# Kernel optimization log

Measured on AMD Instinct MI355X. Metric: run time of the kernel, lower is better.

Reference implementation:

```python
import jax, jax.numpy as jnp
import numpy as np

D_MODEL = 512
NUM_HEADS = 8
HEAD_DIM = D_MODEL // NUM_HEADS
B, L = 2, 4096


def setup_inputs() -> dict:
    key = jax.random.key(0)
    ks = jax.random.split(key, 7)
    query = jax.random.normal(ks[0], (B, L, D_MODEL), dtype=jnp.float32)
    k_in = jax.random.normal(ks[1], (B, L, D_MODEL), dtype=jnp.float32)
    value = jax.random.normal(ks[2], (B, L, D_MODEL), dtype=jnp.float32)
    # causal mask: True = masked (future positions)
    mask = jnp.triu(jnp.ones((L, L), dtype=jnp.bool_), k=1)
    s = 1.0 / np.sqrt(D_MODEL)
    Wq = jax.random.normal(ks[3], (D_MODEL, D_MODEL), dtype=jnp.float32) * s
    Wk = jax.random.normal(ks[4], (D_MODEL, D_MODEL), dtype=jnp.float32) * s
    Wv = jax.random.normal(ks[5], (D_MODEL, D_MODEL), dtype=jnp.float32) * s
    Wo = jax.random.normal(ks[6], (D_MODEL, D_MODEL), dtype=jnp.float32) * s
    return {"query": query, "key": k_in, "value": value, "mask": mask,
            "Wq": Wq, "Wk": Wk, "Wv": Wv, "Wo": Wo}


def reference(query, key, value, mask, Wq, Wk, Wv, Wo):
    b = query.shape[0]
    # torch nn.Linear: y = x @ W.T (no bias)
    q = query @ Wq.T
    k = key @ Wk.T
    v = value @ Wv.T
    q = q.reshape(b, -1, NUM_HEADS, HEAD_DIM)
    k = k.reshape(b, -1, NUM_HEADS, HEAD_DIM)
    v = v.reshape(b, -1, NUM_HEADS, HEAD_DIM)
    logits = jnp.einsum('bqhd,bkhd->bhqk', q, k)  # (B,H,L,L)
    logits = jnp.where(mask, -jnp.inf, logits)
    # NOTE: original scales by 1/sqrt(d_model) (not head_dim), after masking
    attn = jax.nn.softmax(logits / np.sqrt(D_MODEL).astype(np.float32), axis=3)
    out = jnp.einsum('bhqv,bvhd->bqhd', attn, v).reshape(b, -1, D_MODEL)
    return out
```

## Files before the change

kernel.cpp:

```cpp
#include <hip/hip_runtime.h>
#include <hip/hip_bf16.h>
#include <cstdint>

#define DEVI static __device__ __forceinline__

typedef __bf16 bf16x8 __attribute__((ext_vector_type(8)));
typedef float f32x4 __attribute__((ext_vector_type(4)));
typedef float f32x16 __attribute__((ext_vector_type(16)));
typedef unsigned short u16x8 __attribute__((ext_vector_type(8)));

constexpr int Bb = 2, Ll = 4096, Dd = 512, Hh = 8;
constexpr int Mm = Bb * Ll;
constexpr float SCALE2 = 1.4426950408889634f / 22.627416997969522f;
constexpr float MFIX = 16.0f;

constexpr int PITCH = 72;
constexpr int PITCHB = 144;

DEVI unsigned short f2b(float x) {
  __hip_bfloat16 h = __float2bfloat16(x);
  return *reinterpret_cast<unsigned short*>(&h);
}

DEVI float nexp2(float x) { return __builtin_amdgcn_exp2f(x); }

DEVI unsigned cvtpk(float lo, float hi) {
  unsigned r;
  asm("v_cvt_pk_bf16_f32 %0, %1, %2" : "=v"(r) : "v"(lo), "v"(hi));
  return r;
}

DEVI void gll16(const void* g, void* l) {
  __builtin_amdgcn_global_load_lds((const __attribute__((address_space(1))) void*)g,
                                   (__attribute__((address_space(3))) void*)l, 16, 0, 0);
}

__global__ void __launch_bounds__(256, 2) gemm_qkv(const float* __restrict__ Xq,
                                                   const float* __restrict__ Xk,
                                                   const float* __restrict__ Xv,
                                                   const float* __restrict__ Wqp,
                                                   const float* __restrict__ Wkp,
                                                   const float* __restrict__ Wvp,
                                                   unsigned short* __restrict__ Cb,
                                                   unsigned short* __restrict__ VtOut) {
  __shared__ __align__(16) unsigned short As[128 * PITCH];
  __shared__ __align__(16) unsigned short Bs[128 * PITCH];
  const int t = threadIdx.x, lane = t & 63;
  const int w = t >> 6, wm = w >> 1, wn = w & 1;
  const int c = lane & 15, g = lane >> 4;
  const int z = blockIdx.y;
  const float* A = (z == 0) ? Xq : (z == 1) ? Xk : Xv;
  const float* W = (z == 0) ? Wqp : (z == 1) ? Wkp : Wvp;
  const int tm = (blockIdx.x >> 2) * 128;
  const int tn = (blockIdx.x & 3) * 128;
  const int r0 = t >> 3, c8 = t & 7;

  f32x4 acc[4][4] = {};
  for (int k0 = 0; k0 < Dd; k0 += 64) {
#pragma unroll
    for (int u = 0; u < 4; ++u) {
      int r = u * 32 + r0;
      const float4* ap = reinterpret_cast<const float4*>(A + (size_t)(tm + r) * Dd + k0 + c8 * 8);
      const float4* wp = reinterpret_cast<const float4*>(W + (size_t)(tn + r) * Dd + k0 + c8 * 8);
      float4 a0 = ap[0], a1 = ap[1];
      float4 w0 = wp[0], w1 = wp[1];
      uint4 av = make_uint4(cvtpk(a0.x, a0.y), cvtpk(a0.z, a0.w),
                            cvtpk(a1.x, a1.y), cvtpk(a1.z, a1.w));
      uint4 wv = make_uint4(cvtpk(w0.x, w0.y), cvtpk(w0.z, w0.w),
                            cvtpk(w1.x, w1.y), cvtpk(w1.z, w1.w));
      *reinterpret_cast<uint4*>((char*)As + r * PITCHB + c8 * 16) = av;
      *reinterpret_cast<uint4*>((char*)Bs + r * PITCHB + c8 * 16) = wv;
    }
    __syncthreads();
#pragma unroll
    for (int kk = 0; kk < 2; ++kk) {
      bf16x8 af[4], bfv[4];
#pragma unroll
      for (int mi = 0; mi < 4; ++mi) {
        int row = wm * 64 + mi * 16 + c;
        af[mi] = *reinterpret_cast<const bf16x8*>(
            (const char*)As + row * PITCHB + kk * 64 + g * 16);
      }
#pragma unroll
      for (int ni = 0; ni < 4; ++ni) {
        int row = wn * 64 + ni * 16 + c;
        bfv[ni] = *reinterpret_cast<const bf16x8*>(
            (const char*)Bs + row * PITCHB + kk * 64 + g * 16);
      }
#pragma unroll
      for (int mi = 0; mi < 4; ++mi)
#pragma unroll
        for (int ni = 0; ni < 4; ++ni)
          acc[mi][ni] = __builtin_amdgcn_mfma_f32_16x16x32_bf16(af[mi], bfv[ni], acc[mi][ni], 0, 0, 0);
    }
    __syncthreads();
  }
  if (z == 2) {
#pragma unroll
    for (int mi = 0; mi < 4; ++mi) {
      int row0 = tm + wm * 64 + mi * 16 + g * 4;
      int bb = row0 >> 12, l = row0 & 4095;
#pragma unroll
      for (int ni = 0; ni < 4; ++ni) {
        int col = tn + wn * 64 + c + ni * 16;
        uint2 pk = make_uint2(cvtpk(acc[mi][ni][0], acc[mi][ni][1]),
                              cvtpk(acc[mi][ni][2], acc[mi][ni][3]));
        *reinterpret_cast<uint2*>(VtOut + (size_t)(bb * 512 + col) * Ll + l) = pk;
      }
    }
  } else {
    const float scl = (z == 0) ? SCALE2 : 1.0f;
    unsigned short* C = Cb + (size_t)z * (Mm * Dd);
#pragma unroll
    for (int mi = 0; mi < 4; ++mi)
#pragma unroll
      for (int j = 0; j < 4; ++j) {
        size_t row = (size_t)(tm + wm * 64 + mi * 16 + g * 4 + j);
        size_t base = row * Dd + tn + wn * 64 + c;
#pragma unroll
        for (int ni = 0; ni < 4; ++ni) C[base + ni * 16] = f2b(acc[mi][ni][j] * scl);
      }
  }
}

__global__ void __launch_bounds__(256, 2)
attn_kernel(const unsigned short* __restrict__ Q,
            const unsigned short* __restrict__ K,
            const unsigned short* __restrict__ Vt,
            float* __restrict__ O) {
  __shared__ __align__(16) char smem[65536];
  const int t = threadIdx.x, lane = t & 63, w = t >> 6;
  const int g = w >> 1, wq = w & 1;
  const int lq = lane & 31, hi = lane >> 5;
  const int bidx = blockIdx.x;
  const int xg = bidx & 7, rr = bidx >> 3;
  const int half = rr & 1, idx = rr >> 1;
  const int bh = 2 * xg + half;
  const int qi = 63 - idx;
  const int q0 = qi * 64;
  const int b = bh >> 3, h = bh & 7;

  const int qbase = q0 + wq * 32;
  const int qlane = qbase + lq;

  const unsigned short* Qrow = Q + (size_t)(b * Ll + qlane) * Dd + h * 64;
  bf16x8 qf[4];
#pragma unroll
  for (int s = 0; s < 4; ++s)
    qf[s] = *reinterpret_cast<const bf16x8*>(Qrow + s * 16 + hi * 8);

  f32x16 oacc[2] = {};
  float s_r = 0.f;

  const size_t kgbase = (size_t)(b * Ll) * Dd + h * 64;
  const size_t vgbase = (size_t)(bh * 64) * Ll;
  const int nt = qi + 1;
  const int Tg = (nt + 1) >> 1;
  const int kt0 = g * Tg;
  const int lastkt = nt - 1;
  const int ktmax = (qbase + 31) >> 6;
  const int swzl = (lq & 7) << 4;
  const int tg = t & 127;
  const int sK = g * 16384;
  const int sV = 32768 + g * 16384;

  auto STAGE = [&](int par, int kt) {
#pragma unroll
    for (int i = 0; i < 4; ++i) {
      int ch = i * 128 + tg;
      int r = ch >> 3, c8 = ch & 7;
      int srcb = (c8 * 16) ^ ((r & 7) << 4);
      gll16(K + kgbase + (size_t)(kt * 64 + r) * Dd + (srcb >> 1),
            smem + sK + par + r * 128 + c8 * 16);
      gll16(Vt + vgbase + (size_t)r * Ll + kt * 64 + (srcb >> 1),
            smem + sV + par + r * 128 + c8 * 16);
    }
  };

  STAGE(0, kt0 <= lastkt ? kt0 : lastkt);
  for (int j = 0; j < Tg; ++j) {
    const int kt = kt0 + j;
    const int par = (j & 1) * 8192;
    asm volatile("s_waitcnt vmcnt(0)" ::: "memory");
    __builtin_amdgcn_s_barrier();
    if (j + 1 < Tg) {
      int nk = kt + 1 <= lastkt ? kt + 1 : lastkt;
      STAGE(((j + 1) & 1) * 8192, nk);
    }
    __builtin_amdgcn_sched_barrier(0);
    if (kt <= ktmax) {
      const char* Kc = smem + sK + par;
      const char* Vc = smem + sV + par;
      const bool needMask = (kt * 64 + 63 > qbase);
#pragma unroll
      for (int fi = 0; fi < 2; ++fi) {
        f32x16 sacc = {};
        __builtin_amdgcn_s_setprio(1);
#pragma unroll
        for (int s = 0; s < 4; ++s) {
          int off = (s * 32 + hi * 16) ^ swzl;
          bf16x8 kv = *reinterpret_cast<const bf16x8*>(Kc + (lq + 32 * fi) * 128 + off);
          sacc = __builtin_amdgcn_mfma_f32_32x32x16_bf16(kv, qf[s], sacc, 0, 0, 0);
        }
        __builtin_amdgcn_s_setprio(0);
        float p[16];
        if (needMask) {
#pragma unroll
          for (int r = 0; r < 16; ++r) {
            int key = kt * 64 + 32 * fi + (r & 3) + 8 * (r >> 2) + 4 * hi;
            float e = nexp2(sacc[r] - MFIX);
            p[r] = (key > qlane) ? 0.f : e;
          }
        } else {
#pragma unroll
          for (int r = 0; r < 16; ++r) p[r] = nexp2(sacc[r] - MFIX);
        }
        float sm[8];
#pragma unroll
        for (int r = 0; r < 8; ++r) sm[r] = p[r] + p[r + 8];
#pragma unroll
        for (int s = 4; s >= 1; s >>= 1)
#pragma unroll
          for (int r = 0; r < 4; ++r) if (r < s) sm[r] += sm[r + s];
        s_r += sm[0];
        unsigned wpk[4][2];
#pragma unroll
        for (int u = 0; u < 4; ++u) {
          wpk[u][0] = cvtpk(p[4 * u + 0], p[4 * u + 1]);
          wpk[u][1] = cvtpk(p[4 * u + 2], p[4 * u + 3]);
        }
        __builtin_amdgcn_s_setprio(1);
#pragma unroll
        for (int sq = 0; sq < 2; ++sq) {
          const int sp = 2 * fi + sq, u0 = 2 * sq, u1 = u0 + 1;
          unsigned a0 = wpk[u0][0], b0 = wpk[u1][0];
          unsigned a1 = wpk[u0][1], b1 = wpk[u1][1];
          asm("v_permlane32_swap_b32 %0, %1" : "+v"(a0), "+v"(b0));
          asm("v_permlane32_swap_b32 %0, %1" : "+v"(a1), "+v"(b1));
          uint4 bdw = make_uint4(a0, a1, b0, b1);
          bf16x8 bp = *reinterpret_cast<bf16x8*>(&bdw);
          int off = (sp * 32 + hi * 16) ^ swzl;
          bf16x8 v0 = *reinterpret_cast<const bf16x8*>(Vc + lq * 128 + off);
          bf16x8 v1 = *reinterpret_cast<const bf16x8*>(Vc + (lq + 32) * 128 + off);
          oacc[0] = __builtin_amdgcn_mfma_f32_32x32x16_bf16(v0, bp, oacc[0], 0, 0, 0);
          oacc[1] = __builtin_amdgcn_mfma_f32_32x32x16_bf16(v1, bp, oacc[1], 0, 0, 0);
        }
        __builtin_amdgcn_s_setprio(0);
      }
    }
  }
  asm volatile("s_waitcnt vmcnt(0)" ::: "memory");
  __syncthreads();
  const float s_tot = s_r + __shfl_xor(s_r, 32);
  float* eb = reinterpret_cast<float*>(smem);
  const int prow = g * 64 + wq * 32 + lq;
#pragma unroll
  for (int fo = 0; fo < 2; ++fo)
#pragma unroll
    for (int u = 0; u < 4; ++u) {
      int dh = 32 * fo + 8 * u + 4 * hi;
      float4 v4 = make_float4(oacc[fo][4 * u + 0], oacc[fo][4 * u + 1],
                              oacc[fo][4 * u + 2], oacc[fo][4 * u + 3]);
      *reinterpret_cast<float4*>(&eb[prow * 68 + dh]) = v4;
    }
  eb[prow * 68 + 64] = s_tot;
  __syncthreads();
  const int row = t >> 2, q4 = t & 3;
  const float s1 = eb[row * 68 + 64];
  const float s2 = eb[(64 + row) * 68 + 64];
  const float inv = 1.0f / (s1 + s2);
  float* orow = O + (size_t)(b * Ll + q0 + row) * Dd + h * 64 + q4 * 16;
#pragma unroll
  for (int jj = 0; jj < 4; ++jj) {
    float4 o1 = *reinterpret_cast<const float4*>(&eb[row * 68 + q4 * 16 + jj * 4]);
    float4 o2 = *reinterpret_cast<const float4*>(&eb[(64 + row) * 68 + q4 * 16 + jj * 4]);
    float4 o;
    o.x = (o1.x + o2.x) * inv;
    o.y = (o1.y + o2.y) * inv;
    o.z = (o1.z + o2.z) * inv;
    o.w = (o1.w + o2.w) * inv;
    *reinterpret_cast<float4*>(orow + jj * 4) = o;
  }
}

extern "C" void kernel_launch(void* const* d_in, const int* in_sizes, int n_in,
                              void* d_out, int out_size, void* d_ws, size_t ws_size,
                              hipStream_t stream) {
  const float* query = (const float*)d_in[0];
  const float* key   = (const float*)d_in[1];
  const float* value = (const float*)d_in[2];
  const float* Wq = (const float*)d_in[4];
  const float* Wk = (const float*)d_in[5];
  const float* Wv = (const float*)d_in[6];

  unsigned short* QKV = (unsigned short*)d_ws;
  unsigned short* Vt  = QKV + (size_t)3 * Mm * Dd;

  gemm_qkv<<<dim3(256, 3), 256, 0, stream>>>(query, key, value, Wq, Wk, Wv, QKV, Vt);

  unsigned short* Qb = QKV;
  unsigned short* Kb = QKV + (size_t)Mm * Dd;
  attn_kernel<<<1024, 256, 0, stream>>>(Qb, Kb, Vt, (float*)d_out);
}
```

Measured before the change: 95.91 us.

## Stage K/V tiles through registers into single-buffered LDS instead of direct-to-LDS loads

Replaces global_load_lds double buffering of K and V tiles with register prefetch: the next tile is loaded into registers, then written to a single LDS buffer with the XOR swizzle after a barrier. This halves the shared-memory footprint of the attention kernel (from 64KB to about 34KB), which could allow more resident blocks. In exchange it adds an extra barrier per iteration, extra VGPRs for the staged data, and explicit LDS write instructions.

```diff
diff --git a/kernel.cpp b/kernel.cpp
--- a/kernel.cpp
+++ b/kernel.cpp
@@ -28,11 +28,6 @@
   unsigned r;
   asm("v_cvt_pk_bf16_f32 %0, %1, %2" : "=v"(r) : "v"(lo), "v"(hi));
   return r;
-}
-
-DEVI void gll16(const void* g, void* l) {
-  __builtin_amdgcn_global_load_lds((const __attribute__((address_space(1))) void*)g,
-                                   (__attribute__((address_space(3))) void*)l, 16, 0, 0);
 }
 
 __global__ void __launch_bounds__(256, 2) gemm_qkv(const float* __restrict__ Xq,
@@ -128,7 +123,7 @@
             const unsigned short* __restrict__ K,
             const unsigned short* __restrict__ Vt,
             float* __restrict__ O) {
-  __shared__ __align__(16) char smem[65536];
+  __shared__ __align__(16) char smem[34816];
   const int t = threadIdx.x, lane = t & 63, w = t >> 6;
   const int g = w >> 1, wq = w & 1;
   const int lq = lane & 31, hi = lane >> 5;
@@ -161,36 +156,45 @@
   const int ktmax = (qbase + 31) >> 6;
   const int swzl = (lq & 7) << 4;
   const int tg = t & 127;
-  const int sK = g * 16384;
-  const int sV = 32768 + g * 16384;
-
-  auto STAGE = [&](int par, int kt) {
+  const int sK = g * 8192;
+  const int sV = 16384 + g * 8192;
+
+  uint4 kq[4], vq[4];
+  auto LOADT = [&](int kt) {
 #pragma unroll
     for (int i = 0; i < 4; ++i) {
       int ch = i * 128 + tg;
       int r = ch >> 3, c8 = ch & 7;
-      int srcb = (c8 * 16) ^ ((r & 7) << 4);
-      gll16(K + kgbase + (size_t)(kt * 64 + r) * Dd + (srcb >> 1),
-            smem + sK + par + r * 128 + c8 * 16);
-      gll16(Vt + vgbase + (size_t)r * Ll + kt * 64 + (srcb >> 1),
-            smem + sV + par + r * 128 + c8 * 16);
+      kq[i] = *reinterpret_cast<const uint4*>(K + kgbase + (size_t)(kt * 64 + r) * Dd + c8 * 8);
+      vq[i] = *reinterpret_cast<const uint4*>(Vt + vgbase + (size_t)r * Ll + kt * 64 + c8 * 8);
     }
   };
-
-  STAGE(0, kt0 <= lastkt ? kt0 : lastkt);
+  auto WRITET = [&]() {
+#pragma unroll
+    for (int i = 0; i < 4; ++i) {
+      int ch = i * 128 + tg;
+      int r = ch >> 3, c8 = ch & 7;
+      int dst = r * 128 + ((c8 * 16) ^ ((r & 7) << 4));
+      *reinterpret_cast<uint4*>(smem + sK + dst) = kq[i];
+      *reinterpret_cast<uint4*>(smem + sV + dst) = vq[i];
+    }
+  };
+
+  LOADT(kt0 <= lastkt ? kt0 : lastkt);
   for (int j = 0; j < Tg; ++j) {
     const int kt = kt0 + j;
-    const int par = (j & 1) * 8192;
     asm volatile("s_waitcnt vmcnt(0)" ::: "memory");
     __builtin_amdgcn_s_barrier();
+    WRITET();
+    __syncthreads();
     if (j + 1 < Tg) {
       int nk = kt + 1 <= lastkt ? kt + 1 : lastkt;
-      STAGE(((j + 1) & 1) * 8192, nk);
+      LOADT(nk);
     }
     __builtin_amdgcn_sched_barrier(0);
     if (kt <= ktmax) {
-      const char* Kc = smem + sK + par;
-      const char* Vc = smem + sV + par;
+      const char* Kc = smem + sK;
+      const char* Vc = smem + sV;
       const bool needMask = (kt * 64 + 63 > qbase);
 #pragma unroll
       for (int fi = 0; fi < 2; ++fi) {
```

After: 202.9 us. +111.6%, slower.
